# Kernel optimization log

Measured on AMD Instinct MI355X. Metric: run time of the kernel, lower is better.

The kernel has to match this reference:

```python
import jax, jax.numpy as jnp
import numpy as np

EPS = 1e-12  # torch F.normalize eps

def _l2norm(x, axis):
    n = jnp.sqrt(jnp.sum(x * x, axis=axis, keepdims=True))
    return x / jnp.maximum(n, EPS)

def setup_inputs() -> dict:
    key = jax.random.key(0)
    k1, k2, k3, k4 = jax.random.split(key, 4)
    B, Lq, Ld, D, NWAY = 128, 32, 180, 128, 8
    query_reps = jax.random.normal(k1, (B, Lq, D), dtype=jnp.float32)
    doc_reps = jax.random.normal(k2, (B, NWAY, Ld, D), dtype=jnp.float32)
    doc_mask = jax.random.randint(k3, (B, NWAY, Ld), 0, 2, dtype=jnp.int32)
    # labels are teacher log-probabilities (KLDivLoss log_target=True)
    labels = jax.nn.log_softmax(jax.random.normal(k4, (B, NWAY), dtype=jnp.float32), axis=-1)
    return {"query_reps": query_reps, "doc_reps": doc_reps, "doc_mask": doc_mask, "labels": labels}

def reference(query_reps, doc_reps, doc_mask, labels):
    # query: L2-normalize over feature dim (dim=2 in torch call)
    q = _l2norm(query_reps, axis=-1)                      # [B, Lq, D]
    # docs: mask padding tokens, then F.normalize with DEFAULT dim=1,
    # i.e. L2-normalize along the token axis (faithful to source).
    d = doc_reps * doc_mask[..., None].astype(doc_reps.dtype)  # [B, W, Ld, D]
    d = _l2norm(d, axis=2)
    # MaxSim: sim[b,w,q,l] = <q_bq, d_bwl>; max over doc tokens, sum over query tokens
    sim = jnp.einsum('bqd,bwld->bwql', q, d)              # [B, W, Lq, Ld]
    scores = jnp.max(sim, axis=-1).sum(axis=-1)           # [B, W]
    log_p = jax.nn.log_softmax(scores, axis=-1)           # == log(softmax(scores))
    # KLDivLoss(log_target=True, reduction='batchmean'): sum(exp(t)*(t - x)) / B
    B = scores.shape[0]
    loss = jnp.sum(jnp.exp(labels) * (labels - log_p)) / B
    return loss  # torch.mean of a scalar is the scalar
```

## Files before the change

### kernel.cpp

```cpp
#include <hip/hip_runtime.h>
#include <math.h>

#define NB 128
#define LQ 32
#define LD 180
#define DD 128
#define NW 8
#define NBW (NB*NW)
#define TP 36

__global__ __launch_bounds__(256) void qnorm_kernel(
    const float* __restrict__ qreps, float* __restrict__ qinv)
{
    const int t = threadIdx.x, b = blockIdx.x;
    const int r = t >> 3, sub = t & 7;
    const float4* qr = (const float4*)(qreps + (size_t)b * LQ * DD + r * DD + sub * 16);
    float ss = 0.f;
    #pragma unroll
    for (int k = 0; k < 4; ++k) {
        float4 v = qr[k];
        ss += v.x * v.x + v.y * v.y + v.z * v.z + v.w * v.w;
    }
    ss += __shfl_xor(ss, 4);
    ss += __shfl_xor(ss, 2);
    ss += __shfl_xor(ss, 1);
    if (sub == 0) qinv[b * LQ + r] = 1.0f / fmaxf(sqrtf(ss), 1e-12f);
}

__global__ __launch_bounds__(128, 2) void maxsim_kernel(
    const float* __restrict__ qreps, const float* __restrict__ dreps,
    const int* __restrict__ dmask, const float* __restrict__ qinv,
    float* __restrict__ scores)
{
    __shared__ float s_tile[LD * TP];
    __shared__ float s_q[LQ * TP];
    __shared__ float s_ssq[16 * 32];
    __shared__ float s_dinv[32];
    __shared__ float s_pm[2][LQ];

    const int t = threadIdx.x, bw = blockIdx.x, b = bw >> 3;
    const int lane = t & 63, wave = t >> 6;
    const int rowg = lane >> 4;
    const int colg = lane & 15;
    const int colbase = wave * 84;

    const float4* doc4  = (const float4*)(dreps + (size_t)bw * LD * DD);
    const float4* q4g   = (const float4*)(qreps + (size_t)b * LQ * DD);
    const float*  qinvb = qinv + b * LQ;
    const int*    mrow  = dmask + bw * LD;

    const int d4 = t & 7;
    const int rbase = t >> 3;

    float mk[12];
    #pragma unroll
    for (int s = 0; s < 12; ++s) {
        int l = rbase + 16 * s;
        mk[s] = (l < LD) ? (float)mrow[l] : 0.0f;
    }

    float acc[8][6];
    #pragma unroll
    for (int k = 0; k < 8; ++k)
        #pragma unroll
        for (int c = 0; c < 6; ++c) acc[k][c] = 0.f;

    for (int cc = 0; cc < 4; ++cc) {
        if (cc) __syncthreads();

        {
            #pragma unroll
            for (int s = 0; s < 2; ++s) {
                int r = rbase + 16 * s;
                float4 v = q4g[r * 32 + cc * 8 + d4];
                float qi = qinvb[r];
                v.x *= qi; v.y *= qi; v.z *= qi; v.w *= qi;
                *(float4*)&s_q[r * TP + 4 * d4] = v;
            }
        }
        float4 pssq = make_float4(0.f, 0.f, 0.f, 0.f);
        #pragma unroll
        for (int s = 0; s < 12; ++s) {
            int l = rbase + 16 * s;
            if (s < 11 || t < 32) {
                float4 v = doc4[l * 32 + cc * 8 + d4];
                float m = mk[s];
                v.x *= m; v.y *= m; v.z *= m; v.w *= m;
                pssq.x += v.x * v.x; pssq.y += v.y * v.y;
                pssq.z += v.z * v.z; pssq.w += v.w * v.w;
                *(float4*)&s_tile[l * TP + 4 * d4] = v;
            }
        }
        *(float4*)&s_ssq[rbase * 32 + 4 * d4] = pssq;
        __syncthreads();

        if (t < 32) {
            float tot = 0.f;
            #pragma unroll
            for (int g = 0; g < 16; ++g) tot += s_ssq[g * 32 + t];
            s_dinv[t] = 1.0f / fmaxf(sqrtf(tot), 1e-12f);
        }
        __syncthreads();

        {
            float4 di = *(const float4*)&s_dinv[4 * d4];
            #pragma unroll
            for (int s = 0; s < 2; ++s) {
                int r = rbase + 16 * s;
                float4 v = *(float4*)&s_q[r * TP + 4 * d4];
                v.x *= di.x; v.y *= di.y; v.z *= di.z; v.w *= di.w;
                *(float4*)&s_q[r * TP + 4 * d4] = v;
            }
        }
        __syncthreads();

        #pragma unroll
        for (int dq = 0; dq < 8; ++dq) {
            float4 qv[8], tv[6];
            #pragma unroll
            for (int k = 0; k < 8; ++k)
                qv[k] = *(const float4*)&s_q[(rowg + 4 * k) * TP + 4 * dq];
            #pragma unroll
            for (int c = 0; c < 6; ++c)
                tv[c] = *(const float4*)&s_tile[(colbase + colg + 16 * c) * TP + 4 * dq];
            #pragma unroll
            for (int k = 0; k < 8; ++k)
                #pragma unroll
                for (int c = 0; c < 6; ++c) {
                    acc[k][c] = fmaf(qv[k].x, tv[c].x, acc[k][c]);
                    acc[k][c] = fmaf(qv[k].y, tv[c].y, acc[k][c]);
                    acc[k][c] = fmaf(qv[k].z, tv[c].z, acc[k][c]);
                    acc[k][c] = fmaf(qv[k].w, tv[c].w, acc[k][c]);
                }
        }
    }

    float pm[8];
    #pragma unroll
    for (int k = 0; k < 8; ++k) {
        float m = acc[k][0];
        #pragma unroll
        for (int c = 1; c < 6; ++c) m = fmaxf(m, acc[k][c]);
        pm[k] = m;
    }
    #pragma unroll
    for (int off = 8; off >= 1; off >>= 1)
        #pragma unroll
        for (int k = 0; k < 8; ++k)
            pm[k] = fmaxf(pm[k], __shfl_xor(pm[k], off));
    if (colg == 0) {
        #pragma unroll
        for (int k = 0; k < 8; ++k) s_pm[wave][rowg + 4 * k] = pm[k];
    }
    __syncthreads();
    if (t < LQ) {
        float v = fmaxf(s_pm[0][t], s_pm[1][t]);
        #pragma unroll
        for (int off = 16; off >= 1; off >>= 1) v += __shfl_xor(v, off);
        if (t == 0) scores[bw] = v;
    }
}

__global__ __launch_bounds__(NB) void finish_kernel(
    const float* __restrict__ scores, const float* __restrict__ labels,
    float* __restrict__ out)
{
    __shared__ float s_part[2];
    const int t = threadIdx.x;
    const float* sr = scores + t * NW;
    const float* lr = labels + t * NW;

    float s[NW];
    float m = -INFINITY;
    #pragma unroll
    for (int w = 0; w < NW; ++w) { s[w] = sr[w]; m = fmaxf(m, s[w]); }
    float se = 0.f;
    #pragma unroll
    for (int w = 0; w < NW; ++w) se += expf(s[w] - m);
    float lse = logf(se) + m;

    float term = 0.f;
    #pragma unroll
    for (int w = 0; w < NW; ++w) {
        float lw = lr[w];
        term += expf(lw) * (lw - (s[w] - lse));
    }
    #pragma unroll
    for (int off = 32; off > 0; off >>= 1) term += __shfl_xor(term, off);
    if ((t & 63) == 0) s_part[t >> 6] = term;
    __syncthreads();
    if (t == 0) out[0] = (s_part[0] + s_part[1]) / (float)NB;
}

extern "C" void kernel_launch(void* const* d_in, const int* in_sizes, int n_in,
                              void* d_out, int out_size, void* d_ws, size_t ws_size,
                              hipStream_t stream) {
    const float* qreps  = (const float*)d_in[0];
    const float* dreps  = (const float*)d_in[1];
    const int*   dmask  = (const int*)d_in[2];
    const float* labels = (const float*)d_in[3];
    float* out = (float*)d_out;

    float* scores = (float*)d_ws;
    float* qinv   = scores + NBW;

    qnorm_kernel<<<NB, 256, 0, stream>>>(qreps, qinv);
    maxsim_kernel<<<NBW, 128, 0, stream>>>(qreps, dreps, dmask, qinv, scores);
    finish_kernel<<<1, NB, 0, stream>>>(scores, labels, out);
}
```

Before: 180.9 us.

## Compute MaxSim dot products with split-bf16 MFMA and 256-thread blocks

Replaces the scalar FP32 FMA inner product with 32x32x16 bf16 MFMA instructions. Both operands are split into high and low bf16 parts and combined with three MFMAs, which approximates FP32 accuracy. Block size doubles to 256 threads so that four waves share the doc tile and loading and normalisation work. The intent is to move the compute-bound part onto matrix cores; the risks are the bf16x3 precision loss and extra conversion work during tile loading.

After: 156.9 us. 1.15x faster.

```diff
diff --git a/kernel.cpp b/kernel.cpp
--- a/kernel.cpp
+++ b/kernel.cpp
@@ -1,5 +1,6 @@
 #include <hip/hip_runtime.h>
 #include <math.h>
+#include <stdint.h>
 
 #define NB 128
 #define LQ 32
@@ -7,7 +8,20 @@
 #define DD 128
 #define NW 8
 #define NBW (NB*NW)
-#define TP 36
+#define PB 40
+#define LROWS 192
+
+typedef __attribute__((ext_vector_type(8)))  short short8v;
+typedef __attribute__((ext_vector_type(16))) float f32x16;
+
+static __device__ __forceinline__ short bf16_rne(float f) {
+    uint32_t u = __float_as_uint(f);
+    uint32_t r = (u + 0x7fffu + ((u >> 16) & 1u)) >> 16;
+    return (short)r;
+}
+static __device__ __forceinline__ float bf16_f32(short h) {
+    return __uint_as_float(((uint32_t)(uint16_t)h) << 16);
+}
 
 __global__ __launch_bounds__(256) void qnorm_kernel(
     const float* __restrict__ qreps, float* __restrict__ qinv)
@@ -27,68 +41,69 @@
     if (sub == 0) qinv[b * LQ + r] = 1.0f / fmaxf(sqrtf(ss), 1e-12f);
 }
 
-__global__ __launch_bounds__(128, 2) void maxsim_kernel(
+__global__ __launch_bounds__(256, 4) void maxsim_kernel(
     const float* __restrict__ qreps, const float* __restrict__ dreps,
     const int* __restrict__ dmask, const float* __restrict__ qinv,
     float* __restrict__ scores)
 {
-    __shared__ float s_tile[LD * TP];
-    __shared__ float s_q[LQ * TP];
-    __shared__ float s_ssq[16 * 32];
+    __shared__ short s_dh[LROWS * PB];
+    __shared__ short s_dl[LROWS * PB];
+    __shared__ short s_qh[LQ * PB];
+    __shared__ short s_ql[LQ * PB];
+    __shared__ float s_ssq[32 * 32];
     __shared__ float s_dinv[32];
-    __shared__ float s_pm[2][LQ];
+    __shared__ float s_pm[4][LQ];
 
     const int t = threadIdx.x, bw = blockIdx.x, b = bw >> 3;
     const int lane = t & 63, wave = t >> 6;
-    const int rowg = lane >> 4;
-    const int colg = lane & 15;
-    const int colbase = wave * 84;
+    const int d4 = t & 7;
+    const int rbase = t >> 3;
+    const int lh = lane >> 5;
+    const int l31 = lane & 31;
 
     const float4* doc4  = (const float4*)(dreps + (size_t)bw * LD * DD);
     const float4* q4g   = (const float4*)(qreps + (size_t)b * LQ * DD);
     const float*  qinvb = qinv + b * LQ;
     const int*    mrow  = dmask + bw * LD;
 
-    const int d4 = t & 7;
-    const int rbase = t >> 3;
-
-    float mk[12];
-    #pragma unroll
-    for (int s = 0; s < 12; ++s) {
-        int l = rbase + 16 * s;
+    float mk[6];
+    #pragma unroll
+    for (int s = 0; s < 6; ++s) {
+        int l = rbase + 32 * s;
         mk[s] = (l < LD) ? (float)mrow[l] : 0.0f;
     }
 
-    float acc[8][6];
-    #pragma unroll
-    for (int k = 0; k < 8; ++k)
-        #pragma unroll
-        for (int c = 0; c < 6; ++c) acc[k][c] = 0.f;
+    f32x16 acc0 = {};
+    f32x16 acc1 = {};
 
     for (int cc = 0; cc < 4; ++cc) {
         if (cc) __syncthreads();
 
-        {
-            #pragma unroll
-            for (int s = 0; s < 2; ++s) {
-                int r = rbase + 16 * s;
-                float4 v = q4g[r * 32 + cc * 8 + d4];
-                float qi = qinvb[r];
-                v.x *= qi; v.y *= qi; v.z *= qi; v.w *= qi;
-                *(float4*)&s_q[r * TP + 4 * d4] = v;
-            }
-        }
+        float4 qv = q4g[rbase * 32 + cc * 8 + d4];
+
         float4 pssq = make_float4(0.f, 0.f, 0.f, 0.f);
         #pragma unroll
-        for (int s = 0; s < 12; ++s) {
-            int l = rbase + 16 * s;
-            if (s < 11 || t < 32) {
+        for (int s = 0; s < 6; ++s) {
+            int l = rbase + 32 * s;
+            if (l < LD) {
                 float4 v = doc4[l * 32 + cc * 8 + d4];
                 float m = mk[s];
                 v.x *= m; v.y *= m; v.z *= m; v.w *= m;
                 pssq.x += v.x * v.x; pssq.y += v.y * v.y;
                 pssq.z += v.z * v.z; pssq.w += v.w * v.w;
-                *(float4*)&s_tile[l * TP + 4 * d4] = v;
+                short4 h, lo;
+                h.x = bf16_rne(v.x); h.y = bf16_rne(v.y);
+                h.z = bf16_rne(v.z); h.w = bf16_rne(v.w);
+                lo.x = bf16_rne(v.x - bf16_f32(h.x));
+                lo.y = bf16_rne(v.y - bf16_f32(h.y));
+                lo.z = bf16_rne(v.z - bf16_f32(h.z));
+                lo.w = bf16_rne(v.w - bf16_f32(h.w));
+                *(short4*)&s_dh[l * PB + 4 * d4] = h;
+                *(short4*)&s_dl[l * PB + 4 * d4] = lo;
+            } else {
+                short4 z = make_short4(0, 0, 0, 0);
+                *(short4*)&s_dh[l * PB + 4 * d4] = z;
+                *(short4*)&s_dl[l * PB + 4 * d4] = z;
             }
         }
         *(float4*)&s_ssq[rbase * 32 + 4 * d4] = pssq;
@@ -97,64 +112,71 @@
         if (t < 32) {
             float tot = 0.f;
             #pragma unroll
-            for (int g = 0; g < 16; ++g) tot += s_ssq[g * 32 + t];
+            for (int g = 0; g < 32; ++g) tot += s_ssq[g * 32 + t];
             s_dinv[t] = 1.0f / fmaxf(sqrtf(tot), 1e-12f);
         }
         __syncthreads();
 
         {
+            float qi = qinvb[rbase];
             float4 di = *(const float4*)&s_dinv[4 * d4];
-            #pragma unroll
-            for (int s = 0; s < 2; ++s) {
-                int r = rbase + 16 * s;
-                float4 v = *(float4*)&s_q[r * TP + 4 * d4];
-                v.x *= di.x; v.y *= di.y; v.z *= di.z; v.w *= di.w;
-                *(float4*)&s_q[r * TP + 4 * d4] = v;
+            qv.x *= qi * di.x; qv.y *= qi * di.y;
+            qv.z *= qi * di.z; qv.w *= qi * di.w;
+            short4 h, lo;
+            h.x = bf16_rne(qv.x); h.y = bf16_rne(qv.y);
+            h.z = bf16_rne(qv.z); h.w = bf16_rne(qv.w);
+            lo.x = bf16_rne(qv.x - bf16_f32(h.x));
+            lo.y = bf16_rne(qv.y - bf16_f32(h.y));
+            lo.z = bf16_rne(qv.z - bf16_f32(h.z));
+            lo.w = bf16_rne(qv.w - bf16_f32(h.w));
+            *(short4*)&s_qh[rbase * PB + 4 * d4] = h;
+            *(short4*)&s_ql[rbase * PB + 4 * d4] = lo;
+        }
+        __syncthreads();
+
+        #pragma unroll
+        for (int kk = 0; kk < 2; ++kk) {
+            const int ao = l31 * PB + 16 * kk + 8 * lh;
+            short8v ah = *(const short8v*)&s_qh[ao];
+            short8v al = *(const short8v*)&s_ql[ao];
+            const int bo0 = (32 * wave + l31) * PB + 16 * kk + 8 * lh;
+            short8v bh = *(const short8v*)&s_dh[bo0];
+            short8v bl = *(const short8v*)&s_dl[bo0];
+            acc0 = __builtin_amdgcn_mfma_f32_32x32x16_bf16(ah, bh, acc0, 0, 0, 0);
+            acc0 = __builtin_amdgcn_mfma_f32_32x32x16_bf16(ah, bl, acc0, 0, 0, 0);
+            acc0 = __builtin_amdgcn_mfma_f32_32x32x16_bf16(al, bh, acc0, 0, 0, 0);
+            if (wave < 2) {
+                const int bo1 = (32 * (wave + 4) + l31) * PB + 16 * kk + 8 * lh;
+                short8v bh1 = *(const short8v*)&s_dh[bo1];
+                short8v bl1 = *(const short8v*)&s_dl[bo1];
+                acc1 = __builtin_amdgcn_mfma_f32_32x32x16_bf16(ah, bh1, acc1, 0, 0, 0);
+                acc1 = __builtin_amdgcn_mfma_f32_32x32x16_bf16(ah, bl1, acc1, 0, 0, 0);
+                acc1 = __builtin_amdgcn_mfma_f32_32x32x16_bf16(al, bh1, acc1, 0, 0, 0);
             }
         }
-        __syncthreads();
-
-        #pragma unroll
-        for (int dq = 0; dq < 8; ++dq) {
-            float4 qv[8], tv[6];
-            #pragma unroll
-            for (int k = 0; k < 8; ++k)
-                qv[k] = *(const float4*)&s_q[(rowg + 4 * k) * TP + 4 * dq];
-            #pragma unroll
-            for (int c = 0; c < 6; ++c)
-                tv[c] = *(const float4*)&s_tile[(colbase + colg + 16 * c) * TP + 4 * dq];
-            #pragma unroll
-            for (int k = 0; k < 8; ++k)
-                #pragma unroll
-                for (int c = 0; c < 6; ++c) {
-                    acc[k][c] = fmaf(qv[k].x, tv[c].x, acc[k][c]);
-                    acc[k][c] = fmaf(qv[k].y, tv[c].y, acc[k][c]);
-                    acc[k][c] = fmaf(qv[k].z, tv[c].z, acc[k][c]);
-                    acc[k][c] = fmaf(qv[k].w, tv[c].w, acc[k][c]);
-                }
-        }
-    }
-
-    float pm[8];
-    #pragma unroll
-    for (int k = 0; k < 8; ++k) {
-        float m = acc[k][0];
-        #pragma unroll
-        for (int c = 1; c < 6; ++c) m = fmaxf(m, acc[k][c]);
-        pm[k] = m;
-    }
-    #pragma unroll
-    for (int off = 8; off >= 1; off >>= 1)
-        #pragma unroll
-        for (int k = 0; k < 8; ++k)
-            pm[k] = fmaxf(pm[k], __shfl_xor(pm[k], off));
-    if (colg == 0) {
-        #pragma unroll
-        for (int k = 0; k < 8; ++k) s_pm[wave][rowg + 4 * k] = pm[k];
+    }
+
+    float pm[16];
+    #pragma unroll
+    for (int r = 0; r < 16; ++r) {
+        float v = acc0[r];
+        if (wave < 2) v = fmaxf(v, acc1[r]);
+        pm[r] = v;
+    }
+    #pragma unroll
+    for (int off = 1; off <= 16; off <<= 1)
+        #pragma unroll
+        for (int r = 0; r < 16; ++r)
+            pm[r] = fmaxf(pm[r], __shfl_xor(pm[r], off));
+    if (l31 == 0) {
+        #pragma unroll
+        for (int r = 0; r < 16; ++r)
+            s_pm[wave][(r & 3) + 8 * (r >> 2) + 4 * lh] = pm[r];
     }
     __syncthreads();
     if (t < LQ) {
-        float v = fmaxf(s_pm[0][t], s_pm[1][t]);
+        float v = fmaxf(fmaxf(s_pm[0][t], s_pm[1][t]),
+                        fmaxf(s_pm[2][t], s_pm[3][t]));
         #pragma unroll
         for (int off = 16; off >= 1; off >>= 1) v += __shfl_xor(v, off);
         if (t == 0) scores[bw] = v;
@@ -205,6 +227,6 @@
     float* qinv   = scores + NBW;
 
     qnorm_kernel<<<NB, 256, 0, stream>>>(qreps, qinv);
-    maxsim_kernel<<<NBW, 128, 0, stream>>>(qreps, dreps, dmask, qinv, scores);
+    maxsim_kernel<<<NBW, 256, 0, stream>>>(qreps, dreps, dmask, qinv, scores);
     finish_kernel<<<1, NB, 0, stream>>>(scores, labels, out);
 }
```
